# Optimization experiments

Measured on AMD Instinct MI355X. Metric: run time of the kernel, lower is better.

## Reference

```python
import jax, jax.numpy as jnp
import numpy as np

B = 64        # number of graphs
NPG = 4096    # nodes per graph (equal-size segments, batch ids sorted)
H = 256       # hidden_dim
C0, C1 = 256, 64  # num_clusters


def setup_inputs() -> dict:
    key = jax.random.key(0)
    ks = jax.random.split(key, 8)
    N = B * NPG
    x = jax.random.normal(ks[0], (N, H), dtype=jnp.float32)
    edge_index = jax.random.randint(ks[1], (2, N), 0, N, dtype=jnp.int64)  # unused by forward
    batch = jnp.repeat(jnp.arange(B, dtype=jnp.int64), NPG)  # sorted, equal-size segments
    s = 1.0 / np.sqrt(H)
    W0 = jax.random.uniform(ks[2], (H, C0), jnp.float32, -s, s)
    b0 = jax.random.uniform(ks[3], (C0,), jnp.float32, -s, s)
    W1 = jax.random.uniform(ks[4], (H, C1), jnp.float32, -s, s)
    b1 = jax.random.uniform(ks[5], (C1,), jnp.float32, -s, s)
    sf = 1.0 / np.sqrt(C1 * H)
    Wf = jax.random.uniform(ks[6], (C1 * H, H), jnp.float32, -sf, sf)
    bf = jax.random.uniform(ks[7], (H,), jnp.float32, -sf, sf)
    return {"x": x, "edge_index": edge_index, "batch": batch,
            "W0": W0, "b0": b0, "W1": W1, "b1": b1, "Wf": Wf, "bf": bf}


def reference(x, edge_index, batch, W0, b0, W1, b1, Wf, bf):
    # Level 0: softmax cluster assignment + per-graph segmented matmul A^T @ F.
    # batch ids are sorted with equal-size segments, so the per-graph Python
    # loop of the original collapses to a reshape + batched einsum.
    A0 = jax.nn.softmax(x @ W0 + b0, axis=-1)                      # [N, C0]
    f0 = jnp.einsum('bnc,bnh->bch',
                    A0.reshape(B, NPG, C0),
                    x.reshape(B, NPG, H)).reshape(B * C0, H)        # [B*C0, H]
    # Level 1: same pattern on pooled cluster features (C0 'nodes' per graph).
    A1 = jax.nn.softmax(f0 @ W1 + b1, axis=-1)                     # [B*C0, C1]
    f1 = jnp.einsum('bnc,bnh->bch',
                    A1.reshape(B, C0, C1),
                    f0.reshape(B, C0, H)).reshape(B, C1 * H)        # [B, C1*H]
    # Final pool: Linear -> ReLU (Dropout is identity in eval mode).
    return jax.nn.relu(f1 @ Wf + bf)                               # [B, H]
```

## Files before the change

### kernel.cpp

```cpp
#include <hip/hip_runtime.h>
#include <stdint.h>

#define NG   64
#define NPG  4096
#define HD   256
#define NC0  256
#define NC1  64
#define KSPLIT 2

typedef __attribute__((ext_vector_type(8))) short bfx8;
typedef __attribute__((ext_vector_type(4))) float fx4;

__device__ __forceinline__ unsigned short f2bf(float f) {
  union { float f; unsigned int u; } v; v.f = f;
  return (unsigned short)((v.u + 0x7FFFu + ((v.u >> 16) & 1u)) >> 16);
}
__device__ __forceinline__ unsigned int pack2(float a, float b) {
  return (unsigned int)f2bf(a) | ((unsigned int)f2bf(b) << 16);
}

#define ASYNC_COPY16(gptr, lptr) \
  __builtin_amdgcn_global_load_lds((const __attribute__((address_space(1))) unsigned int*)(gptr), \
                                   (__attribute__((address_space(3))) unsigned int*)(lptr), 16, 0, 0)

__global__ __launch_bounds__(256) void k_w0f(const float* __restrict__ W0,
                                             unsigned short* __restrict__ W0F) {
  int gid = blockIdx.x * 256 + threadIdx.x;
  int l15 = gid & 15;
  int q   = (gid >> 4) & 3;
  int ks  = (gid >> 6) & 1;
  int kc  = (gid >> 7) & 3;
  int cblk = gid >> 9;
  int c = cblk * 16 + l15;
  int kb = kc * 64 + ks * 32 + q * 8;
  unsigned int u[4];
  #pragma unroll
  for (int j = 0; j < 8; j += 2)
    u[j >> 1] = pack2(W0[(size_t)(kb + j) * 256 + c], W0[(size_t)(kb + j + 1) * 256 + c]);
  *(float4*)(W0F + (size_t)gid * 8) = *(float4*)u;
}

__global__ __launch_bounds__(256, 4) void k_assign0(
    const float* __restrict__ x, const unsigned short* __restrict__ W0F,
    const float* __restrict__ b0, unsigned short* __restrict__ A0T,
    unsigned short* __restrict__ xT, int g0) {
  __shared__ unsigned short lds_u[9216];
  __shared__ float red[64 * 4];

  int gl = blockIdx.x >> 6, nt = blockIdx.x & 63;
  int tid = threadIdx.x;
  int wn = tid >> 6, lane = tid & 63;
  int l15 = lane & 15, q = lane >> 4;

  fx4 acc[4][4];
  #pragma unroll
  for (int i = 0; i < 4; ++i)
    #pragma unroll
    for (int j = 0; j < 4; ++j) acc[i][j] = fx4{0.f, 0.f, 0.f, 0.f};

  const float* xbase = x + ((size_t)(g0 + gl) * NPG + (size_t)nt * 64) * HD;
  int snode = tid >> 2, sseg = (tid & 3) * 16;
  int sg0  = sseg >> 3;
  int sswz = (snode ^ (snode >> 4)) & 7;

  {
    const float4* src = (const float4*)(xbase + (size_t)snode * HD + sseg);
    float4 v0 = src[0], v1 = src[1], v2 = src[2], v3 = src[3];
    float4 pv[2]; unsigned int* pu = (unsigned int*)pv;
    pu[0] = pack2(v0.x, v0.y); pu[1] = pack2(v0.z, v0.w);
    pu[2] = pack2(v1.x, v1.y); pu[3] = pack2(v1.z, v1.w);
    pu[4] = pack2(v2.x, v2.y); pu[5] = pack2(v2.z, v2.w);
    pu[6] = pack2(v3.x, v3.y); pu[7] = pack2(v3.z, v3.w);
    unsigned short* drow = &lds_u[snode << 6];
    *(float4*)(drow + ((sg0 ^ sswz) << 3))       = pv[0];
    *(float4*)(drow + (((sg0 + 1) ^ sswz) << 3)) = pv[1];
  }
  __syncthreads();

  for (int kc = 0; kc < 4; ++kc) {
    int buf = kc & 1;
    const unsigned short* xb = &lds_u[buf * 4096];
    float4 v0, v1, v2, v3;
    if (kc < 3) {
      const float4* src = (const float4*)(xbase + (size_t)snode * HD + (kc + 1) * 64 + sseg);
      v0 = src[0]; v1 = src[1]; v2 = src[2]; v3 = src[3];
    }
    #pragma unroll
    for (int ks = 0; ks < 2; ++ks) {
      bfx8 af[4];
      #pragma unroll
      for (int mi = 0; mi < 4; ++mi) {
        int slot = (ks * 4 + q) ^ (l15 & 7) ^ mi;
        af[mi] = *(const bfx8*)&xb[((mi * 16 + l15) << 6) + (slot << 3)];
      }
      #pragma unroll
      for (int ni = 0; ni < 4; ++ni) {
        bfx8 bv = *(const bfx8*)(W0F + ((size_t)(((wn * 4 + ni) * 8 + kc * 2 + ks) * 64 + lane)) * 8);
        #pragma unroll
        for (int mi = 0; mi < 4; ++mi)
          acc[mi][ni] = __builtin_amdgcn_mfma_f32_16x16x32_bf16(af[mi], bv, acc[mi][ni], 0, 0, 0);
      }
    }
    {
      int hl = tid >> 2, s4 = tid & 3, sg = s4 * 16;
      int gcol = hl >> 3, off = hl & 7;
      unsigned int u[8];
      #pragma unroll
      for (int i = 0; i < 16; i += 2) {
        int r0 = sg + i;
        unsigned short a = xb[(r0 << 6)       + ((gcol ^ (i & 7)       ^ s4) << 3) + off];
        unsigned short b = xb[((r0 + 1) << 6) + ((gcol ^ ((i + 1) & 7) ^ s4) << 3) + off];
        u[i >> 1] = (unsigned int)a | ((unsigned int)b << 16);
      }
      float4* dst = (float4*)(xT + ((size_t)gl * HD + kc * 64 + hl) * NPG + (size_t)nt * 64 + sg);
      dst[0] = *(float4*)&u[0];
      dst[1] = *(float4*)&u[4];
    }
    if (kc < 3) {
      float4 pv[2]; unsigned int* pu = (unsigned int*)pv;
      pu[0] = pack2(v0.x, v0.y); pu[1] = pack2(v0.z, v0.w);
      pu[2] = pack2(v1.x, v1.y); pu[3] = pack2(v1.z, v1.w);
      pu[4] = pack2(v2.x, v2.y); pu[5] = pack2(v2.z, v2.w);
      pu[6] = pack2(v3.x, v3.y); pu[7] = pack2(v3.z, v3.w);
      unsigned short* drow = &lds_u[((buf ^ 1) * 4096) + (snode << 6)];
      *(float4*)(drow + ((sg0 ^ sswz) << 3))       = pv[0];
      *(float4*)(drow + (((sg0 + 1) ^ sswz) << 3)) = pv[1];
    }
    __syncthreads();
  }

  float bv4[4];
  #pragma unroll
  for (int ni = 0; ni < 4; ++ni) bv4[ni] = b0[wn * 64 + ni * 16 + l15];
  #pragma unroll
  for (int mi = 0; mi < 4; ++mi)
    #pragma unroll
    for (int ni = 0; ni < 4; ++ni)
      #pragma unroll
      for (int r = 0; r < 4; ++r) acc[mi][ni][r] += bv4[ni];

  float mrow[4][4];
  #pragma unroll
  for (int mi = 0; mi < 4; ++mi)
    #pragma unroll
    for (int r = 0; r < 4; ++r) {
      float m = fmaxf(fmaxf(acc[mi][0][r], acc[mi][1][r]), fmaxf(acc[mi][2][r], acc[mi][3][r]));
      #pragma unroll
      for (int off = 1; off < 16; off <<= 1) m = fmaxf(m, __shfl_xor(m, off));
      mrow[mi][r] = m;
    }
  if (l15 == 0) {
    #pragma unroll
    for (int mi = 0; mi < 4; ++mi)
      #pragma unroll
      for (int r = 0; r < 4; ++r)
        red[(mi * 16 + q * 4 + r) * 4 + wn] = mrow[mi][r];
  }
  __syncthreads();
  #pragma unroll
  for (int mi = 0; mi < 4; ++mi)
    #pragma unroll
    for (int r = 0; r < 4; ++r) {
      float4 rv = *(const float4*)&red[(mi * 16 + q * 4 + r) * 4];
      mrow[mi][r] = fmaxf(fmaxf(rv.x, rv.y), fmaxf(rv.z, rv.w));
    }
  __syncthreads();
  float srow[4][4];
  #pragma unroll
  for (int mi = 0; mi < 4; ++mi)
    #pragma unroll
    for (int r = 0; r < 4; ++r) {
      float s = 0.f;
      #pragma unroll
      for (int ni = 0; ni < 4; ++ni) {
        float e = __expf(acc[mi][ni][r] - mrow[mi][r]);
        acc[mi][ni][r] = e; s += e;
      }
      #pragma unroll
      for (int off = 1; off < 16; off <<= 1) s += __shfl_xor(s, off);
      srow[mi][r] = s;
    }
  if (l15 == 0) {
    #pragma unroll
    for (int mi = 0; mi < 4; ++mi)
      #pragma unroll
      for (int r = 0; r < 4; ++r)
        red[(mi * 16 + q * 4 + r) * 4 + wn] = srow[mi][r];
  }
  __syncthreads();
  #pragma unroll
  for (int mi = 0; mi < 4; ++mi)
    #pragma unroll
    for (int r = 0; r < 4; ++r) {
      float4 rv = *(const float4*)&red[(mi * 16 + q * 4 + r) * 4];
      float inv = 1.f / (rv.x + rv.y + rv.z + rv.w);
      #pragma unroll
      for (int ni = 0; ni < 4; ++ni) acc[mi][ni][r] *= inv;
    }
  __syncthreads();

  unsigned short* at = lds_u;
  unsigned short* A0Tg = A0T + (size_t)gl * NC0 * NPG + (size_t)nt * 64;
  #pragma unroll
  for (int p = 0; p < 2; ++p) {
    if ((wn >> 1) == p) {
      int cb = (wn & 1) * 64;
      #pragma unroll
      for (int mi = 0; mi < 4; ++mi) {
        int ncol = mi * 16 + q * 4;
        #pragma unroll
        for (int ni = 0; ni < 4; ++ni) {
          int cl = cb + ni * 16 + l15;
          uint2 w;
          w.x = pack2(acc[mi][ni][0], acc[mi][ni][1]);
          w.y = pack2(acc[mi][ni][2], acc[mi][ni][3]);
          *(uint2*)(at + cl * 72 + ncol) = w;
        }
      }
    }
    __syncthreads();
    {
      int row = tid >> 1, sg2 = (tid & 1) * 32;
      const float4* s4p = (const float4*)(at + row * 72 + sg2);
      float4 a = s4p[0], b = s4p[1], c = s4p[2], d = s4p[3];
      float4* d4 = (float4*)(A0Tg + (size_t)(p * 128 + row) * NPG + sg2);
      d4[0] = a; d4[1] = b; d4[2] = c; d4[3] = d;
    }
    __syncthreads();
  }
}

__global__ __launch_bounds__(256, 2) void k_pool0(
    const unsigned short* __restrict__ A0T, const unsigned short* __restrict__ xT,
    float* __restrict__ f0p, int g0) {
  __shared__ unsigned short a_s[128 * 64];
  __shared__ unsigned short b_s[128 * 64];
  int bid = blockIdx.x;
  int kidx = bid & 1;
  int nt = (bid >> 1) & 1;
  int mt = (bid >> 2) & 1;
  int gl = bid >> 3;

  int tid = threadIdx.x;
  int wave = tid >> 6, lane = tid & 63;
  int wm = wave >> 1, wnn = wave & 1;
  int l15 = lane & 15, q = lane >> 4;

  const int KPER = NPG / KSPLIT;
  const unsigned short* abase = A0T + ((size_t)gl * NC0 + (size_t)mt * 128) * NPG + (size_t)kidx * KPER;
  const unsigned short* bbase = xT  + ((size_t)gl * HD  + (size_t)nt * 128) * NPG + (size_t)kidx * KPER;

  fx4 acc[4][4];
  #pragma unroll
  for (int i = 0; i < 4; ++i)
    #pragma unroll
    for (int j = 0; j < 4; ++j) acc[i][j] = fx4{0.f, 0.f, 0.f, 0.f};

  int srow = lane >> 3;
  int sg   = (lane & 7) ^ srow;
  size_t soff = (size_t)srow * NPG + (size_t)sg * 8;

  for (int k0 = 0; k0 < KPER; k0 += 64) {
    #pragma unroll
    for (int i = 0; i < 4; ++i) {
      int r0 = wave * 32 + i * 8;
      ASYNC_COPY16(abase + (size_t)r0 * NPG + k0 + soff, &a_s[r0 * 64]);
      ASYNC_COPY16(bbase + (size_t)r0 * NPG + k0 + soff, &b_s[r0 * 64]);
    }
    __syncthreads();
    #pragma unroll
    for (int ks = 0; ks < 2; ++ks) {
      int gx = ((ks * 4 + q) ^ (l15 & 7)) << 3;
      bfx8 af[4], bf[4];
      #pragma unroll
      for (int mi = 0; mi < 4; ++mi)
        af[mi] = *(const bfx8*)&a_s[(wm * 64 + mi * 16 + l15) * 64 + gx];
      #pragma unroll
      for (int ni = 0; ni < 4; ++ni)
        bf[ni] = *(const bfx8*)&b_s[(wnn * 64 + ni * 16 + l15) * 64 + gx];
      #pragma unroll
      for (int ni = 0; ni < 4; ++ni)
        #pragma unroll
        for (int mi = 0; mi < 4; ++mi)
          acc[mi][ni] = __builtin_amdgcn_mfma_f32_16x16x32_bf16(af[mi], bf[ni], acc[mi][ni], 0, 0, 0);
    }
    __syncthreads();
  }

  float* dst = f0p + (size_t)kidx * NG * NC0 * HD
             + ((size_t)(g0 + gl) * NC0 + (size_t)mt * 128) * HD + (size_t)nt * 128;
  #pragma unroll
  for (int mi = 0; mi < 4; ++mi)
    #pragma unroll
    for (int ni = 0; ni < 4; ++ni) {
      int c = wm * 64 + mi * 16 + q * 4;
      int h = wnn * 64 + ni * 16 + l15;
      #pragma unroll
      for (int r = 0; r < 4; ++r)
        dst[(size_t)(c + r) * HD + h] = acc[mi][ni][r];
    }
}

__global__ __launch_bounds__(256) void k_f0sum(float* __restrict__ f0) {
  size_t i = ((size_t)blockIdx.x * 256 + threadIdx.x) * 4;
  float4 a = *(const float4*)(f0 + i);
  float4 b = *(const float4*)(f0 + (size_t)NG * NC0 * HD + i);
  a.x += b.x; a.y += b.y; a.z += b.z; a.w += b.w;
  *(float4*)(f0 + i) = a;
}

__global__ __launch_bounds__(256) void k_assign1(
    const float* __restrict__ f0, const float* __restrict__ W1,
    const float* __restrict__ b1, float* __restrict__ A1) {
  __shared__ float w1s[256 * 64];
  int tid = threadIdx.x;
  #pragma unroll
  for (int i = 0; i < 16; ++i) {
    int off = i * 1024 + tid * 4;
    *(float4*)(w1s + off) = *(const float4*)(W1 + off);
  }
  __syncthreads();
  int lane = tid & 63;
  int rbase = blockIdx.x * 32 + (tid >> 6) * 8;
  float bias = b1[lane];
  for (int rr = 0; rr < 8; ++rr) {
    int row = rbase + rr;
    const float* fr = f0 + (size_t)row * 256;
    float acc = bias;
    for (int k = 0; k < 256; k += 4) {
      float4 fv = *(const float4*)(fr + k);
      acc += fv.x * w1s[(k    ) * 64 + lane];
      acc += fv.y * w1s[(k + 1) * 64 + lane];
      acc += fv.z * w1s[(k + 2) * 64 + lane];
      acc += fv.w * w1s[(k + 3) * 64 + lane];
    }
    float m = acc;
    #pragma unroll
    for (int off = 1; off < 64; off <<= 1) m = fmaxf(m, __shfl_xor(m, off));
    float e = __expf(acc - m);
    float s = e;
    #pragma unroll
    for (int off = 1; off < 64; off <<= 1) s += __shfl_xor(s, off);
    A1[(size_t)row * 64 + lane] = e / s;
  }
}

__global__ __launch_bounds__(256) void k_pool1(
    const float* __restrict__ A1, const float* __restrict__ f0, float* __restrict__ f1) {
  int b = blockIdx.x >> 2, cg = blockIdx.x & 3;
  int h = threadIdx.x;
  const float* a1p = A1 + (size_t)b * NC0 * NC1 + cg * 16;
  const float* f0p = f0 + (size_t)b * NC0 * HD + h;
  float acc[16];
  #pragma unroll
  for (int j = 0; j < 16; ++j) acc[j] = 0.f;
  for (int c0 = 0; c0 < 256; ++c0) {
    float fv = f0p[(size_t)c0 * 256];
    #pragma unroll
    for (int j = 0; j < 16; ++j) acc[j] += a1p[c0 * 64 + j] * fv;
  }
  float* d = f1 + (size_t)b * 16384 + (size_t)(cg * 16) * 256 + h;
  #pragma unroll
  for (int j = 0; j < 16; ++j) d[(size_t)j * 256] = acc[j];
}

__global__ __launch_bounds__(512) void k_final_partial(
    const float* __restrict__ f1, const float* __restrict__ Wf, float* __restrict__ ot) {
  __shared__ float f1s[64 * 256];
  int ht = blockIdx.x & 3;
  int ks = blockIdx.x >> 2;
  int tid = threadIdx.x;
  {
    int b = tid >> 3, c0 = (tid & 7) * 4;
    const float* s = f1 + (size_t)b * 16384 + (size_t)ks * 256 + c0;
    float* d = f1s + b * 256 + c0;
    #pragma unroll
    for (int i = 0; i < 8; ++i) *(float4*)(d + i * 32) = *(const float4*)(s + i * 32);
  }
  __syncthreads();
  int h = ht * 64 + (tid & 63);
  int b0 = (tid >> 6) * 8;
  const float* wp = Wf + (size_t)ks * 256 * 256 + h;
  float acc[8];
  #pragma unroll
  for (int j = 0; j < 8; ++j) acc[j] = 0.f;
  for (int k = 0; k < 256; k += 4) {
    float w0 = wp[(size_t)(k    ) * 256];
    float w1 = wp[(size_t)(k + 1) * 256];
    float w2 = wp[(size_t)(k + 2) * 256];
    float w3 = wp[(size_t)(k + 3) * 256];
    #pragma unroll
    for (int j = 0; j < 8; ++j) {
      float4 fv = *(const float4*)(f1s + (b0 + j) * 256 + k);
      acc[j] += fv.x * w0 + fv.y * w1 + fv.z * w2 + fv.w * w3;
    }
  }
  #pragma unroll
  for (int j = 0; j < 8; ++j) atomicAdd(&ot[(b0 + j) * 256 + h], acc[j]);
}

__global__ __launch_bounds__(256) void k_final_out(
    const float* __restrict__ ot, const float* __restrict__ bfv, float* __restrict__ out) {
  int i = blockIdx.x * 256 + threadIdx.x;
  float v = ot[i] + bfv[i & 255];
  out[i] = v > 0.f ? v : 0.f;
}

extern "C" void kernel_launch(void* const* d_in, const int* in_sizes, int n_in,
                              void* d_out, int out_size, void* d_ws, size_t ws_size,
                              hipStream_t stream) {
  const float* x   = (const float*)d_in[0];
  const float* W0  = (const float*)d_in[3];
  const float* b0  = (const float*)d_in[4];
  const float* W1  = (const float*)d_in[5];
  const float* b1  = (const float*)d_in[6];
  const float* Wf  = (const float*)d_in[7];
  const float* bfv = (const float*)d_in[8];
  float* out = (float*)d_out;
  char* ws = (char*)d_ws;

  float* f0p = (float*)ws;
  float* f0  = f0p;
  float* ot  = (float*)(ws + ((size_t)32 << 20));
  unsigned short* W0F = (unsigned short*)(ws + ((size_t)32 << 20) + 65536);
  size_t chunk_off = ((size_t)32 << 20) + 65536 + 131072;
  size_t per_graph = (size_t)4 * HD * NPG;
  size_t avail = ws_size > chunk_off ? ws_size - chunk_off : 0;
  int G = (int)(avail / per_graph);
  if (G > 64) G = 64;
  if (G < 1) G = 1;
  unsigned short* xT  = (unsigned short*)(ws + chunk_off);
  unsigned short* A0T = xT + (size_t)G * HD * NPG;
  float* f1 = (float*)xT;
  float* A1 = (float*)A0T;

  hipMemsetAsync(ot, 0, 65536, stream);
  k_w0f<<<32, 256, 0, stream>>>(W0, W0F);

  for (int g0 = 0; g0 < NG; g0 += G) {
    int gc = (NG - g0 < G) ? (NG - g0) : G;
    k_assign0<<<gc * 64, 256, 0, stream>>>(x, W0F, b0, A0T, xT, g0);
    k_pool0<<<gc * 4 * KSPLIT, 256, 0, stream>>>(A0T, xT, f0p, g0);
  }
  k_f0sum<<<4096, 256, 0, stream>>>(f0);
  k_assign1<<<512, 256, 0, stream>>>(f0, W1, b1, A1);
  k_pool1<<<256, 256, 0, stream>>>(A1, f0, f1);
  k_final_partial<<<256, 512, 0, stream>>>(f1, Wf, ot);
  k_final_out<<<64, 256, 0, stream>>>(ot, bfv, out);
}
```

Before: 692.7 us.

## Double k_assign0 tile to 128 nodes with 512 threads and prefetch W0 fragments

k_assign0 now processes 128 nodes per block with 8 waves arranged 2x4, so each W0 fragment loaded from global serves twice as many rows and the block count halves. W0F fragments are software-prefetched one k-step ahead into registers, and the xT transpose store and A0T writeback are reorganized into per-wave 16-byte row-contiguous writes with a row-dependent LDS swizzle. The cost is more LDS per block (about 37KB) and more registers, which may reduce occupancy at launch_bounds(512,4).

```diff
diff --git a/kernel.cpp b/kernel.cpp
--- a/kernel.cpp
+++ b/kernel.cpp
@@ -40,16 +40,17 @@
   *(float4*)(W0F + (size_t)gid * 8) = *(float4*)u;
 }
 
-__global__ __launch_bounds__(256, 4) void k_assign0(
+__global__ __launch_bounds__(512, 4) void k_assign0(
     const float* __restrict__ x, const unsigned short* __restrict__ W0F,
     const float* __restrict__ b0, unsigned short* __restrict__ A0T,
     unsigned short* __restrict__ xT, int g0) {
-  __shared__ unsigned short lds_u[9216];
-  __shared__ float red[64 * 4];
-
-  int gl = blockIdx.x >> 6, nt = blockIdx.x & 63;
+  __shared__ unsigned short lds_u[18432];
+  __shared__ float red[512];
+
+  int gl = blockIdx.x >> 5, nt = blockIdx.x & 31;
   int tid = threadIdx.x;
-  int wn = tid >> 6, lane = tid & 63;
+  int wave = tid >> 6, lane = tid & 63;
+  int wm = wave >> 2, wn = wave & 3;
   int l15 = lane & 15, q = lane >> 4;
 
   fx4 acc[4][4];
@@ -58,10 +59,16 @@
     #pragma unroll
     for (int j = 0; j < 4; ++j) acc[i][j] = fx4{0.f, 0.f, 0.f, 0.f};
 
-  const float* xbase = x + ((size_t)(g0 + gl) * NPG + (size_t)nt * 64) * HD;
-  int snode = tid >> 2, sseg = (tid & 3) * 16;
-  int sg0  = sseg >> 3;
-  int sswz = (snode ^ (snode >> 4)) & 7;
+  const float* xbase = x + ((size_t)(g0 + gl) * NPG + (size_t)nt * 128) * HD;
+  int snode = tid >> 2;
+  int sseg  = (tid & 3) * 16;
+  int sg0   = (tid & 3) * 2;
+  int ssw   = (snode ^ (snode >> 4)) & 7;
+
+  bfx8 bvc[4], bvn[4];
+  #pragma unroll
+  for (int ni = 0; ni < 4; ++ni)
+    bvc[ni] = *(const bfx8*)(W0F + ((size_t)(((wn * 4 + ni) * 8 + 0) * 64 + lane)) * 8);
 
   {
     const float4* src = (const float4*)(xbase + (size_t)snode * HD + sseg);
@@ -72,14 +79,14 @@
     pu[4] = pack2(v2.x, v2.y); pu[5] = pack2(v2.z, v2.w);
     pu[6] = pack2(v3.x, v3.y); pu[7] = pack2(v3.z, v3.w);
     unsigned short* drow = &lds_u[snode << 6];
-    *(float4*)(drow + ((sg0 ^ sswz) << 3))       = pv[0];
-    *(float4*)(drow + (((sg0 + 1) ^ sswz) << 3)) = pv[1];
-  }
-  __syncthreads();
-
+    *(float4*)(drow + (((sg0    ) ^ ssw) << 3)) = pv[0];
+    *(float4*)(drow + (((sg0 + 1) ^ ssw) << 3)) = pv[1];
+  }
+  __syncthreads();
+
+  #pragma unroll
   for (int kc = 0; kc < 4; ++kc) {
-    int buf = kc & 1;
-    const unsigned short* xb = &lds_u[buf * 4096];
+    const unsigned short* xb = &lds_u[(kc & 1) * 8192];
     float4 v0, v1, v2, v3;
     if (kc < 3) {
       const float4* src = (const float4*)(xbase + (size_t)snode * HD + (kc + 1) * 64 + sseg);
@@ -87,34 +94,43 @@
     }
     #pragma unroll
     for (int ks = 0; ks < 2; ++ks) {
+      int g8 = kc * 2 + ks;
+      if (g8 < 7) {
+        #pragma unroll
+        for (int ni = 0; ni < 4; ++ni)
+          bvn[ni] = *(const bfx8*)(W0F + ((size_t)(((wn * 4 + ni) * 8 + g8 + 1) * 64 + lane)) * 8);
+      }
       bfx8 af[4];
       #pragma unroll
       for (int mi = 0; mi < 4; ++mi) {
-        int slot = (ks * 4 + q) ^ (l15 & 7) ^ mi;
-        af[mi] = *(const bfx8*)&xb[((mi * 16 + l15) << 6) + (slot << 3)];
-      }
-      #pragma unroll
-      for (int ni = 0; ni < 4; ++ni) {
-        bfx8 bv = *(const bfx8*)(W0F + ((size_t)(((wn * 4 + ni) * 8 + kc * 2 + ks) * 64 + lane)) * 8);
+        int row = wm * 64 + mi * 16 + l15;
+        int slot = (ks * 4 + q) ^ ((row ^ (row >> 4)) & 7);
+        af[mi] = *(const bfx8*)&xb[(row << 6) + (slot << 3)];
+      }
+      #pragma unroll
+      for (int ni = 0; ni < 4; ++ni)
         #pragma unroll
         for (int mi = 0; mi < 4; ++mi)
-          acc[mi][ni] = __builtin_amdgcn_mfma_f32_16x16x32_bf16(af[mi], bv, acc[mi][ni], 0, 0, 0);
-      }
-    }
-    {
-      int hl = tid >> 2, s4 = tid & 3, sg = s4 * 16;
-      int gcol = hl >> 3, off = hl & 7;
-      unsigned int u[8];
-      #pragma unroll
-      for (int i = 0; i < 16; i += 2) {
-        int r0 = sg + i;
-        unsigned short a = xb[(r0 << 6)       + ((gcol ^ (i & 7)       ^ s4) << 3) + off];
-        unsigned short b = xb[((r0 + 1) << 6) + ((gcol ^ ((i + 1) & 7) ^ s4) << 3) + off];
-        u[i >> 1] = (unsigned int)a | ((unsigned int)b << 16);
-      }
-      float4* dst = (float4*)(xT + ((size_t)gl * HD + kc * 64 + hl) * NPG + (size_t)nt * 64 + sg);
-      dst[0] = *(float4*)&u[0];
-      dst[1] = *(float4*)&u[4];
+          acc[mi][ni] = __builtin_amdgcn_mfma_f32_16x16x32_bf16(af[mi], bvc[ni], acc[mi][ni], 0, 0, 0);
+      if (g8 < 7) {
+        #pragma unroll
+        for (int ni = 0; ni < 4; ++ni) bvc[ni] = bvn[ni];
+      }
+    }
+    #pragma unroll
+    for (int p2 = 0; p2 < 2; ++p2) {
+      int hl = p2 * 32 + wave * 4 + (lane >> 4);
+      int g = hl >> 3, off = hl & 7;
+      int nb = (lane & 15) * 8;
+      unsigned int u[4];
+      #pragma unroll
+      for (int j = 0; j < 8; j += 2) {
+        int n0 = nb + j, n1 = n0 + 1;
+        unsigned short a = xb[(n0 << 6) + ((g ^ ((n0 ^ (n0 >> 4)) & 7)) << 3) + off];
+        unsigned short b = xb[(n1 << 6) + ((g ^ ((n1 ^ (n1 >> 4)) & 7)) << 3) + off];
+        u[j >> 1] = (unsigned int)a | ((unsigned int)b << 16);
+      }
+      *(float4*)(xT + ((size_t)gl * HD + kc * 64 + hl) * NPG + (size_t)nt * 128 + nb) = *(float4*)u;
     }
     if (kc < 3) {
       float4 pv[2]; unsigned int* pu = (unsigned int*)pv;
@@ -122,9 +138,9 @@
       pu[2] = pack2(v1.x, v1.y); pu[3] = pack2(v1.z, v1.w);
       pu[4] = pack2(v2.x, v2.y); pu[5] = pack2(v2.z, v2.w);
       pu[6] = pack2(v3.x, v3.y); pu[7] = pack2(v3.z, v3.w);
-      unsigned short* drow = &lds_u[((buf ^ 1) * 4096) + (snode << 6)];
-      *(float4*)(drow + ((sg0 ^ sswz) << 3))       = pv[0];
-      *(float4*)(drow + (((sg0 + 1) ^ sswz) << 3)) = pv[1];
+      unsigned short* drow = &lds_u[(((kc & 1) ^ 1) * 8192) + (snode << 6)];
+      *(float4*)(drow + (((sg0    ) ^ ssw) << 3)) = pv[0];
+      *(float4*)(drow + (((sg0 + 1) ^ ssw) << 3)) = pv[1];
     }
     __syncthreads();
   }
@@ -154,14 +170,14 @@
     for (int mi = 0; mi < 4; ++mi)
       #pragma unroll
       for (int r = 0; r < 4; ++r)
-        red[(mi * 16 + q * 4 + r) * 4 + wn] = mrow[mi][r];
+        red[(wm * 64 + mi * 16 + q * 4 + r) * 4 + wn] = mrow[mi][r];
   }
   __syncthreads();
   #pragma unroll
   for (int mi = 0; mi < 4; ++mi)
     #pragma unroll
     for (int r = 0; r < 4; ++r) {
-      float4 rv = *(const float4*)&red[(mi * 16 + q * 4 + r) * 4];
+      float4 rv = *(const float4*)&red[(wm * 64 + mi * 16 + q * 4 + r) * 4];
       mrow[mi][r] = fmaxf(fmaxf(rv.x, rv.y), fmaxf(rv.z, rv.w));
     }
   __syncthreads();
@@ -185,14 +201,14 @@
     for (int mi = 0; mi < 4; ++mi)
       #pragma unroll
       for (int r = 0; r < 4; ++r)
-        red[(mi * 16 + q * 4 + r) * 4 + wn] = srow[mi][r];
+        red[(wm * 64 + mi * 16 + q * 4 + r) * 4 + wn] = srow[mi][r];
   }
   __syncthreads();
   #pragma unroll
   for (int mi = 0; mi < 4; ++mi)
     #pragma unroll
     for (int r = 0; r < 4; ++r) {
-      float4 rv = *(const float4*)&red[(mi * 16 + q * 4 + r) * 4];
+      float4 rv = *(const float4*)&red[(wm * 64 + mi * 16 + q * 4 + r) * 4];
       float inv = 1.f / (rv.x + rv.y + rv.z + rv.w);
       #pragma unroll
       for (int ni = 0; ni < 4; ++ni) acc[mi][ni][r] *= inv;
@@ -200,31 +216,31 @@
   __syncthreads();
 
   unsigned short* at = lds_u;
-  unsigned short* A0Tg = A0T + (size_t)gl * NC0 * NPG + (size_t)nt * 64;
+  unsigned short* A0Tg = A0T + (size_t)gl * NC0 * NPG + (size_t)nt * 128;
   #pragma unroll
   for (int p = 0; p < 2; ++p) {
     if ((wn >> 1) == p) {
       int cb = (wn & 1) * 64;
       #pragma unroll
       for (int mi = 0; mi < 4; ++mi) {
-        int ncol = mi * 16 + q * 4;
+        int ncol = wm * 64 + mi * 16 + q * 4;
         #pragma unroll
         for (int ni = 0; ni < 4; ++ni) {
           int cl = cb + ni * 16 + l15;
           uint2 w;
           w.x = pack2(acc[mi][ni][0], acc[mi][ni][1]);
           w.y = pack2(acc[mi][ni][2], acc[mi][ni][3]);
-          *(uint2*)(at + cl * 72 + ncol) = w;
+          *(uint2*)(at + cl * 144 + ncol) = w;
         }
       }
     }
     __syncthreads();
-    {
-      int row = tid >> 1, sg2 = (tid & 1) * 32;
-      const float4* s4p = (const float4*)(at + row * 72 + sg2);
-      float4 a = s4p[0], b = s4p[1], c = s4p[2], d = s4p[3];
-      float4* d4 = (float4*)(A0Tg + (size_t)(p * 128 + row) * NPG + sg2);
-      d4[0] = a; d4[1] = b; d4[2] = c; d4[3] = d;
+    #pragma unroll
+    for (int rp = 0; rp < 4; ++rp) {
+      int row = rp * 32 + wave * 4 + (lane >> 4);
+      int nb = (lane & 15) * 8;
+      bfx8 vv = *(const bfx8*)(at + row * 144 + nb);
+      *(bfx8*)(A0Tg + (size_t)(p * 128 + row) * NPG + nb) = vv;
     }
     __syncthreads();
   }
@@ -439,7 +455,7 @@
 
   for (int g0 = 0; g0 < NG; g0 += G) {
     int gc = (NG - g0 < G) ? (NG - g0) : G;
-    k_assign0<<<gc * 64, 256, 0, stream>>>(x, W0F, b0, A0T, xT, g0);
+    k_assign0<<<gc * 32, 512, 0, stream>>>(x, W0F, b0, A0T, xT, g0);
     k_pool0<<<gc * 4 * KSPLIT, 256, 0, stream>>>(A0T, xT, f0p, g0);
   }
   k_f0sum<<<4096, 256, 0, stream>>>(f0);
```

New measurement: 735.2 us. 1.06x slower.
